# Kernel optimization log

Measured on AMD Instinct MI355X. Metric: run time of the kernel, lower is better.

## Reference

```python
import jax, jax.numpy as jnp
import numpy as np

B, S, D, H, DH = 8192, 64, 32, 4, 8

def setup_inputs() -> dict:
    key = jax.random.key(0)
    ks = jax.random.split(key, 10)
    lim = 1.0 / np.sqrt(D)
    def lin(k):
        kw, kb = jax.random.split(k)
        W = jax.random.uniform(kw, (D, D), jnp.float32, -lim, lim)
        b = jax.random.uniform(kb, (D,), jnp.float32, -lim, lim)
        return W, b
    Wq, bq = lin(ks[0]); Wk, bk = lin(ks[1]); Wv, bv = lin(ks[2]); Wp, bp = lin(ks[3])
    x = jax.random.normal(ks[4], (B, S, D), jnp.float32)
    always_attend_upto = jax.random.randint(ks[5], (B,), 0, 64, jnp.int64 if jax.config.jax_enable_x64 else jnp.int32)
    return {"x": x, "always_attend_upto": always_attend_upto,
            "Wq": Wq, "bq": bq, "Wk": Wk, "bk": bk, "Wv": Wv, "bv": bv, "Wp": Wp, "bp": bp}

def reference(x, always_attend_upto, Wq, bq, Wk, bk, Wv, bv, Wp, bp):
    # QKV projections (torch Linear: y = x @ W.T + b)
    def heads(W, b):
        y = x @ W.T + b                      # [B,S,D]
        return y.reshape(B, S, H, DH).transpose(0, 2, 1, 3)  # [B,H,S,DH]
    q, k, v = heads(Wq, bq), heads(Wk, bk), heads(Wv, bv)
    score = jnp.einsum('bhqd,bhkd->bhqk', q, k) / jnp.sqrt(jnp.float32(DH))
    # prefix-LM mask: allowed if causal (j<=i) OR key in prefix (j < length[b])
    i = jnp.arange(S)[:, None]
    j = jnp.arange(S)[None, :]
    causal = j <= i                                        # [S,S]
    prefix = j[None, :, :] < always_attend_upto[:, None, None]  # [B,S,S]
    allowed = (causal[None] | prefix)[:, None, :, :]       # [B,1,S,S]
    score = jnp.where(allowed, score, -jnp.inf)
    attn = jax.nn.softmax(score, axis=-1)
    out = jnp.einsum('bhqk,bhkd->bhqd', attn, v)           # [B,H,S,DH]
    out = out.transpose(0, 2, 1, 3).reshape(B, S, D)
    return out @ Wp.T + bp
```

## Files before the change

kernel.cpp:

```cpp
#include <hip/hip_runtime.h>
#include <cstdint>
#include <cstddef>

#define NB 8192

typedef __attribute__((ext_vector_type(8))) short short8;
typedef __attribute__((ext_vector_type(4))) float f32x4;

union S8U { short8 s; unsigned u[4]; uint4 v; };

static __device__ __forceinline__ unsigned pk2(float a, float b) {
    unsigned short ua = __builtin_bit_cast(unsigned short, (__bf16)a);
    unsigned short ub = __builtin_bit_cast(unsigned short, (__bf16)b);
    return (unsigned)ua | ((unsigned)ub << 16);
}

#define MFMA __builtin_amdgcn_mfma_f32_16x16x32_bf16
#define BPERM __builtin_amdgcn_ds_bpermute
#define LDSFENCE() asm volatile("" ::: "memory")

__global__ __launch_bounds__(128, 4) void fused_attn_mfma(
    const float* __restrict__ x,
    const int*   __restrict__ aatt,
    const float* __restrict__ Wq, const float* __restrict__ bq,
    const float* __restrict__ Wk, const float* __restrict__ bk,
    const float* __restrict__ Wv, const float* __restrict__ bv,
    const float* __restrict__ Wp, const float* __restrict__ bp,
    float* __restrict__ out)
{
    __shared__ __align__(16) short klds[64][40];
    __shared__ __align__(16) short vbt[32][72];
    __shared__ __align__(16) short psl[2][16][40];

    const int tid  = threadIdx.x;
    const int w    = tid >> 6;
    const int lane = tid & 63;
    const int q4   = lane >> 4;
    const int l15  = lane & 15;
    const int b    = blockIdx.x;

    const int aab      = aatt[b];
    const unsigned bmask = (q4 == 0) ? 0xFFFFFFFFu : 0u;

    int cmpv[4];
#pragma unroll
    for (int it = 0; it < 4; ++it) cmpv[it] = max(l15 + 16*it, aab - 1) - q4*4;

    short8 xa[4];
    const float* xb = x + (size_t)b * 64 * 32;
#pragma unroll
    for (int nt = 0; nt < 4; ++nt) {
        const float* p = xb + (nt*16 + l15)*32 + q4*8;
        float4 u0 = *(const float4*)p;
        float4 u1 = *(const float4*)(p + 4);
        S8U t;
        t.u[0] = pk2(u0.x, u0.y); t.u[1] = pk2(u0.z, u0.w);
        t.u[2] = pk2(u1.x, u1.y); t.u[3] = pk2(u1.z, u1.w);
        xa[nt] = t.s;
    }

    auto wrow = [&](const float* W, int row) -> short8 {
        const float* p = W + row*32 + q4*8;
        float4 u0 = *(const float4*)p;
        float4 u1 = *(const float4*)(p + 4);
        S8U t;
        t.u[0] = pk2(u0.x, u0.y); t.u[1] = pk2(u0.z, u0.w);
        t.u[2] = pk2(u1.x, u1.y); t.u[3] = pk2(u1.z, u1.w);
        return t.s;
    };

    const float escale = 0.35355339059327373f * 1.4426950408889634f;

    unsigned qpk01[4], qpk23[4];
    {
        short8 wa = wrow(Wq, 16*w + l15);
        float4 b4 = *(const float4*)(bq + 16*w + q4*4);
#pragma unroll
        for (int nt = 0; nt < 4; ++nt) {
            f32x4 acc = {0.f,0.f,0.f,0.f};
            acc = MFMA(wa, xa[nt], acc, 0,0,0);
            qpk01[nt] = pk2((acc[0]+b4.x)*escale, (acc[1]+b4.y)*escale);
            qpk23[nt] = pk2((acc[2]+b4.z)*escale, (acc[3]+b4.w)*escale);
        }
    }
    {
        short8 wa = wrow(Wk, 16*w + l15);
        float4 b4 = *(const float4*)(bk + 16*w + q4*4);
#pragma unroll
        for (int nt = 0; nt < 4; ++nt) {
            f32x4 acc = {0.f,0.f,0.f,0.f};
            acc = MFMA(wa, xa[nt], acc, 0,0,0);
            uint2 w2;
            w2.x = pk2(acc[0]+b4.x, acc[1]+b4.y);
            w2.y = pk2(acc[2]+b4.z, acc[3]+b4.w);
            *(uint2*)&klds[nt*16 + l15][16*w + q4*4] = w2;
        }
    }
    {
        short8 wv = wrow(Wv, 16*w + l15);
        const float bvv = bv[16*w + l15];
#pragma unroll
        for (int mt = 0; mt < 4; ++mt) {
            f32x4 acc = {0.f,0.f,0.f,0.f};
            acc = MFMA(xa[mt], wv, acc, 0,0,0);
            uint2 w2;
            w2.x = pk2(acc[0]+bvv, acc[1]+bvv);
            w2.y = pk2(acc[2]+bvv, acc[3]+bvv);
            *(uint2*)&vbt[16*w + l15][mt*16 + q4*4] = w2;
        }
    }
    LDSFENCE();

    unsigned opk01s[2][4], opk23s[2][4];

#pragma unroll
    for (int hl = 0; hl < 2; ++hl) {
        const int idxA = (32*hl + l15) * 4;
        const int idxB = idxA + 64;

        short8 sqb[4];
#pragma unroll
        for (int it = 0; it < 4; ++it) {
            S8U t;
            t.u[0] = (unsigned)BPERM(idxA, (int)qpk01[it]) & bmask;
            t.u[1] = (unsigned)BPERM(idxA, (int)qpk23[it]) & bmask;
            t.u[2] = (unsigned)BPERM(idxB, (int)qpk01[it]) & bmask;
            t.u[3] = (unsigned)BPERM(idxB, (int)qpk23[it]) & bmask;
            sqb[it] = t.s;
        }

        float csum[4] = {0.f,0.f,0.f,0.f};
        f32x4 oacch[4];
#pragma unroll
        for (int it = 0; it < 4; ++it) oacch[it] = (f32x4){0.f,0.f,0.f,0.f};

#pragma unroll
        for (int jb = 0; jb < 2; ++jb) {
            short8 ska[2];
#pragma unroll
            for (int jt = 0; jt < 2; ++jt) {
                S8U t; t.v = *(const uint4*)&klds[jb*32 + jt*16 + l15][16*w + 8*hl];
                ska[jt] = t.s;
            }
            S8U av; av.v = *(const uint4*)&vbt[16*w + 8*hl + (l15 & 7)][jb*32 + q4*8];

#pragma unroll
            for (int it = 0; it < 4; ++it) {
#pragma unroll
                for (int jt = 0; jt < 2; ++jt) {
                    f32x4 sacc = {0.f,0.f,0.f,0.f};
                    sacc = MFMA(ska[jt], sqb[it], sacc, 0,0,0);
                    float e[4];
#pragma unroll
                    for (int r = 0; r < 4; ++r) {
                        float ee = __builtin_amdgcn_exp2f(sacc[r]);
                        e[r] = (jb*32 + jt*16 + r <= cmpv[it]) ? ee : 0.0f;
                    }
                    csum[it] += (e[0]+e[1]) + (e[2]+e[3]);
                    uint2 pw; pw.x = pk2(e[0], e[1]); pw.y = pk2(e[2], e[3]);
                    *(uint2*)&psl[w][l15][jt*16 + q4*4] = pw;
                }
                LDSFENCE();
                S8U pb; pb.v = *(const uint4*)&psl[w][l15][q4*8];
                oacch[it] = MFMA(av.s, pb.s, oacch[it], 0,0,0);
                LDSFENCE();
            }
        }

        float inv[4];
#pragma unroll
        for (int it = 0; it < 4; ++it) {
            float a = csum[it];
            a += __shfl_xor(a, 16, 64);
            a += __shfl_xor(a, 32, 64);
            inv[it] = 1.0f / a;
        }
#pragma unroll
        for (int it = 0; it < 4; ++it) {
            opk01s[hl][it] = pk2(oacch[it][0]*inv[it], oacch[it][1]*inv[it]);
            opk23s[hl][it] = pk2(oacch[it][2]*inv[it], oacch[it][3]*inv[it]);
        }
    }

    f32x4 yacc[4][2];
#pragma unroll
    for (int mt = 0; mt < 4; ++mt)
#pragma unroll
        for (int nt = 0; nt < 2; ++nt) yacc[mt][nt] = (f32x4){0.f,0.f,0.f,0.f};

    const int idx0 = l15 * 4;
    const int idx1 = idx0 + 64;
#pragma unroll
    for (int hl = 0; hl < 2; ++hl) {
        short8 wpb[2];
#pragma unroll
        for (int nt = 0; nt < 2; ++nt) {
            const float* p = Wp + (nt*16 + l15)*32 + 16*w + 8*hl;
            float4 u0 = *(const float4*)p;
            float4 u1 = *(const float4*)(p + 4);
            S8U t;
            t.u[0] = pk2(u0.x,u0.y) & bmask;
            t.u[1] = pk2(u0.z,u0.w) & bmask;
            t.u[2] = pk2(u1.x,u1.y) & bmask;
            t.u[3] = pk2(u1.z,u1.w) & bmask;
            wpb[nt] = t.s;
        }
#pragma unroll
        for (int mtile = 0; mtile < 4; ++mtile) {
            S8U t;
            t.u[0] = (unsigned)BPERM(idx0, (int)opk01s[hl][mtile]);
            t.u[1] = (unsigned)BPERM(idx0, (int)opk23s[hl][mtile]);
            t.u[2] = (unsigned)BPERM(idx1, (int)opk01s[hl][mtile]);
            t.u[3] = (unsigned)BPERM(idx1, (int)opk23s[hl][mtile]);
#pragma unroll
            for (int nt = 0; nt < 2; ++nt)
                yacc[mtile][nt] = MFMA(t.s, wpb[nt], yacc[mtile][nt], 0,0,0);
        }
    }

    __syncthreads();
    float* scrA = (float*)&klds[0][0];
    float* scrB = (float*)&vbt[0][0];
    if (w == 0) {
#pragma unroll
        for (int mtl = 0; mtl < 2; ++mtl)
#pragma unroll
            for (int nt = 0; nt < 2; ++nt)
                *(f32x4*)&scrA[((mtl*2 + nt)*64 + lane)*4] = yacc[2 + mtl][nt];
    } else {
#pragma unroll
        for (int mtl = 0; mtl < 2; ++mtl)
#pragma unroll
            for (int nt = 0; nt < 2; ++nt)
                *(f32x4*)&scrB[((mtl*2 + nt)*64 + lane)*4] = yacc[mtl][nt];
    }
    __syncthreads();

    const float bpv[2] = { bp[l15], bp[16 + l15] };
    float* ob = out + (size_t)b * 64 * 32;
    if (w == 0) {
#pragma unroll
        for (int mtl = 0; mtl < 2; ++mtl)
#pragma unroll
            for (int nt = 0; nt < 2; ++nt) {
                f32x4 o = *(const f32x4*)&scrB[((mtl*2 + nt)*64 + lane)*4];
#pragma unroll
                for (int r = 0; r < 4; ++r)
                    ob[(mtl*16 + q4*4 + r)*32 + nt*16 + l15] =
                        yacc[mtl][nt][r] + o[r] + bpv[nt];
            }
    } else {
#pragma unroll
        for (int mtl = 0; mtl < 2; ++mtl)
#pragma unroll
            for (int nt = 0; nt < 2; ++nt) {
                f32x4 o = *(const f32x4*)&scrA[((mtl*2 + nt)*64 + lane)*4];
#pragma unroll
                for (int r = 0; r < 4; ++r)
                    ob[((2 + mtl)*16 + q4*4 + r)*32 + nt*16 + l15] =
                        yacc[2 + mtl][nt][r] + o[r] + bpv[nt];
            }
    }
}

extern "C" void kernel_launch(void* const* d_in, const int* in_sizes, int n_in,
                              void* d_out, int out_size, void* d_ws, size_t ws_size,
                              hipStream_t stream) {
    const float* x  = (const float*)d_in[0];
    const int*   aa = (const int*)d_in[1];
    const float* Wq = (const float*)d_in[2];
    const float* bq = (const float*)d_in[3];
    const float* Wk = (const float*)d_in[4];
    const float* bk = (const float*)d_in[5];
    const float* Wv = (const float*)d_in[6];
    const float* bv = (const float*)d_in[7];
    const float* Wp = (const float*)d_in[8];
    const float* bp = (const float*)d_in[9];
    float* out = (float*)d_out;

    dim3 grid(NB), block(128);
    hipLaunchKernelGGL(fused_attn_mfma, grid, block, 0, stream,
                       x, aa, Wq, bq, Wk, bk, Wv, bv, Wp, bp, out);
}
```

Baseline: 62.33 us.

## Fold softmax row-sum into PV MFMA and restructure output projection via LDS

Adds a row of bf16 ones to the V tile, so the unused MFMA rows of the PV product produce the softmax denominator. This removes the per-element csum additions and the cross-lane shuffles. The output projection now stages normalized attention outputs in LDS and runs one full-K MFMA per tile per wave. This replaces the masked per-head partial MFMAs and the cross-wave scratch reduction. The denominator is now accumulated in bf16-rounded probabilities and uses an approximate reciprocal, which may shift accuracy slightly.

```diff
diff --git a/kernel.cpp b/kernel.cpp
--- a/kernel.cpp
+++ b/kernel.cpp
@@ -8,6 +8,7 @@
 typedef __attribute__((ext_vector_type(4))) float f32x4;
 
 union S8U { short8 s; unsigned u[4]; uint4 v; };
+union FI { float f; int i; unsigned u; };
 
 static __device__ __forceinline__ unsigned pk2(float a, float b) {
     unsigned short ua = __builtin_bit_cast(unsigned short, (__bf16)a);
@@ -29,7 +30,7 @@
     float* __restrict__ out)
 {
     __shared__ __align__(16) short klds[64][40];
-    __shared__ __align__(16) short vbt[32][72];
+    __shared__ __align__(16) short vbt[33][72];
     __shared__ __align__(16) short psl[2][16][40];
 
     const int tid  = threadIdx.x;
@@ -39,7 +40,7 @@
     const int l15  = lane & 15;
     const int b    = blockIdx.x;
 
-    const int aab      = aatt[b];
+    const int aab = aatt[b];
     const unsigned bmask = (q4 == 0) ? 0xFFFFFFFFu : 0u;
 
     int cmpv[4];
@@ -109,6 +110,10 @@
             *(uint2*)&vbt[16*w + l15][mt*16 + q4*4] = w2;
         }
     }
+    if (q4 == 0) {
+        uint2 ones; ones.x = 0x3F803F80u; ones.y = 0x3F803F80u;
+        *(uint2*)&vbt[32][l15*4] = ones;
+    }
     LDSFENCE();
 
     unsigned opk01s[2][4], opk23s[2][4];
@@ -129,7 +134,9 @@
             sqb[it] = t.s;
         }
 
-        float csum[4] = {0.f,0.f,0.f,0.f};
+        const int avrow = (l15 < 8) ? (16*w + 8*hl + l15) : 32;
+        const short* avbase = &vbt[avrow][0];
+
         f32x4 oacch[4];
 #pragma unroll
         for (int it = 0; it < 4; ++it) oacch[it] = (f32x4){0.f,0.f,0.f,0.f};
@@ -142,7 +149,7 @@
                 S8U t; t.v = *(const uint4*)&klds[jb*32 + jt*16 + l15][16*w + 8*hl];
                 ska[jt] = t.s;
             }
-            S8U av; av.v = *(const uint4*)&vbt[16*w + 8*hl + (l15 & 7)][jb*32 + q4*8];
+            S8U av; av.v = *(const uint4*)&avbase[jb*32 + q4*8];
 
 #pragma unroll
             for (int it = 0; it < 4; ++it) {
@@ -156,7 +163,6 @@
                         float ee = __builtin_amdgcn_exp2f(sacc[r]);
                         e[r] = (jb*32 + jt*16 + r <= cmpv[it]) ? ee : 0.0f;
                     }
-                    csum[it] += (e[0]+e[1]) + (e[2]+e[3]);
                     uint2 pw; pw.x = pk2(e[0], e[1]); pw.y = pk2(e[2], e[3]);
                     *(uint2*)&psl[w][l15][jt*16 + q4*4] = pw;
                 }
@@ -167,99 +173,44 @@
             }
         }
 
-        float inv[4];
 #pragma unroll
         for (int it = 0; it < 4; ++it) {
-            float a = csum[it];
-            a += __shfl_xor(a, 16, 64);
-            a += __shfl_xor(a, 32, 64);
-            inv[it] = 1.0f / a;
-        }
-#pragma unroll
-        for (int it = 0; it < 4; ++it) {
-            opk01s[hl][it] = pk2(oacch[it][0]*inv[it], oacch[it][1]*inv[it]);
-            opk23s[hl][it] = pk2(oacch[it][2]*inv[it], oacch[it][3]*inv[it]);
-        }
-    }
-
-    f32x4 yacc[4][2];
-#pragma unroll
-    for (int mt = 0; mt < 4; ++mt)
-#pragma unroll
-        for (int nt = 0; nt < 2; ++nt) yacc[mt][nt] = (f32x4){0.f,0.f,0.f,0.f};
-
-    const int idx0 = l15 * 4;
-    const int idx1 = idx0 + 64;
-#pragma unroll
-    for (int hl = 0; hl < 2; ++hl) {
-        short8 wpb[2];
-#pragma unroll
-        for (int nt = 0; nt < 2; ++nt) {
-            const float* p = Wp + (nt*16 + l15)*32 + 16*w + 8*hl;
-            float4 u0 = *(const float4*)p;
-            float4 u1 = *(const float4*)(p + 4);
-            S8U t;
-            t.u[0] = pk2(u0.x,u0.y) & bmask;
-            t.u[1] = pk2(u0.z,u0.w) & bmask;
-            t.u[2] = pk2(u1.x,u1.y) & bmask;
-            t.u[3] = pk2(u1.z,u1.w) & bmask;
-            wpb[nt] = t.s;
-        }
-#pragma unroll
-        for (int mtile = 0; mtile < 4; ++mtile) {
-            S8U t;
-            t.u[0] = (unsigned)BPERM(idx0, (int)opk01s[hl][mtile]);
-            t.u[1] = (unsigned)BPERM(idx0, (int)opk23s[hl][mtile]);
-            t.u[2] = (unsigned)BPERM(idx1, (int)opk01s[hl][mtile]);
-            t.u[3] = (unsigned)BPERM(idx1, (int)opk23s[hl][mtile]);
-#pragma unroll
-            for (int nt = 0; nt < 2; ++nt)
-                yacc[mtile][nt] = MFMA(t.s, wpb[nt], yacc[mtile][nt], 0,0,0);
+            FI s; s.i = BPERM((32 + l15) * 4, __builtin_bit_cast(int, oacch[it][0]));
+            const float inv = __builtin_amdgcn_rcpf(s.f);
+            opk01s[hl][it] = pk2(oacch[it][0]*inv, oacch[it][1]*inv);
+            opk23s[hl][it] = pk2(oacch[it][2]*inv, oacch[it][3]*inv);
         }
     }
 
     __syncthreads();
-    float* scrA = (float*)&klds[0][0];
-    float* scrB = (float*)&vbt[0][0];
-    if (w == 0) {
-#pragma unroll
-        for (int mtl = 0; mtl < 2; ++mtl)
-#pragma unroll
-            for (int nt = 0; nt < 2; ++nt)
-                *(f32x4*)&scrA[((mtl*2 + nt)*64 + lane)*4] = yacc[2 + mtl][nt];
-    } else {
-#pragma unroll
-        for (int mtl = 0; mtl < 2; ++mtl)
-#pragma unroll
-            for (int nt = 0; nt < 2; ++nt)
-                *(f32x4*)&scrB[((mtl*2 + nt)*64 + lane)*4] = yacc[mtl][nt];
+    if (q4 < 2) {
+#pragma unroll
+        for (int hl = 0; hl < 2; ++hl)
+#pragma unroll
+            for (int it = 0; it < 4; ++it) {
+                uint2 ow; ow.x = opk01s[hl][it]; ow.y = opk23s[hl][it];
+                *(uint2*)&klds[it*16 + l15][(2*w + hl)*8 + q4*4] = ow;
+            }
     }
     __syncthreads();
+
+    short8 wpb[2];
+#pragma unroll
+    for (int nt = 0; nt < 2; ++nt) wpb[nt] = wrow(Wp, nt*16 + l15);
 
     const float bpv[2] = { bp[l15], bp[16 + l15] };
     float* ob = out + (size_t)b * 64 * 32;
-    if (w == 0) {
-#pragma unroll
-        for (int mtl = 0; mtl < 2; ++mtl)
-#pragma unroll
-            for (int nt = 0; nt < 2; ++nt) {
-                f32x4 o = *(const f32x4*)&scrB[((mtl*2 + nt)*64 + lane)*4];
-#pragma unroll
-                for (int r = 0; r < 4; ++r)
-                    ob[(mtl*16 + q4*4 + r)*32 + nt*16 + l15] =
-                        yacc[mtl][nt][r] + o[r] + bpv[nt];
-            }
-    } else {
-#pragma unroll
-        for (int mtl = 0; mtl < 2; ++mtl)
-#pragma unroll
-            for (int nt = 0; nt < 2; ++nt) {
-                f32x4 o = *(const f32x4*)&scrA[((mtl*2 + nt)*64 + lane)*4];
-#pragma unroll
-                for (int r = 0; r < 4; ++r)
-                    ob[((2 + mtl)*16 + q4*4 + r)*32 + nt*16 + l15] =
-                        yacc[2 + mtl][nt][r] + o[r] + bpv[nt];
-            }
+#pragma unroll
+    for (int u = 0; u < 2; ++u) {
+        S8U oa; oa.v = *(const uint4*)&klds[(2*w + u)*16 + l15][q4*8];
+#pragma unroll
+        for (int nt = 0; nt < 2; ++nt) {
+            f32x4 y = {0.f,0.f,0.f,0.f};
+            y = MFMA(oa.s, wpb[nt], y, 0,0,0);
+#pragma unroll
+            for (int r = 0; r < 4; ++r)
+                ob[((2*w + u)*16 + q4*4 + r)*32 + nt*16 + l15] = y[r] + bpv[nt];
+        }
     }
 }
 
```

New measurement: 50.69 us. 1.23x faster.
